# Optimization experiments

Measured on AMD Instinct MI355X. Metric: run time of the kernel, lower is better.

## Reference

```python
import jax, jax.numpy as jnp
import numpy as np

GRID_SIZE = 5
SPLINE_ORDER = 3
IN_FEAT = 320   # 32 * 10
OUT_FEAT = 2048 # 32 * 64
BN_EPS = 1e-3


def make_grid():
    # efficient-kan grid buffer: (in_features, grid_size + 2*spline_order + 1)
    h = 2.0 / GRID_SIZE  # grid_range = [-1, 1]
    g = jnp.arange(-SPLINE_ORDER, GRID_SIZE + SPLINE_ORDER + 1, dtype=jnp.float32) * h - 1.0
    return jnp.broadcast_to(g, (IN_FEAT, g.shape[0]))  # (320, 12)


def b_splines(x, grid):
    # x: (B, In) -> bases: (B, In, grid_size + spline_order)
    x = x[..., None]  # (B, In, 1)
    bases = ((x >= grid[:, :-1]) & (x < grid[:, 1:])).astype(x.dtype)
    for k in range(1, SPLINE_ORDER + 1):
        left = (x - grid[:, : -(k + 1)]) / (grid[:, k:-1] - grid[:, : -(k + 1)])
        right = (grid[:, k + 1:] - x) / (grid[:, k + 1:] - grid[:, 1:-k])
        bases = left * bases[..., :-1] + right * bases[..., 1:]
    return bases


def setup_inputs() -> dict:
    key = jax.random.key(0)
    ks = jax.random.split(key, 8)
    N = 40000
    inputs = jax.random.normal(ks[0], (N, 32, 10), dtype=jnp.float32)
    linear_w = jax.random.normal(ks[1], (64, 10), dtype=jnp.float32) * 0.1
    base_weight = jax.random.normal(ks[2], (OUT_FEAT, IN_FEAT), dtype=jnp.float32) * 0.02
    spline_weight = jax.random.normal(ks[3], (OUT_FEAT, IN_FEAT, GRID_SIZE + SPLINE_ORDER), dtype=jnp.float32) * 0.02
    spline_scaler = jax.random.normal(ks[4], (OUT_FEAT, IN_FEAT), dtype=jnp.float32) * 0.1 + 1.0
    bn_gamma = jax.random.normal(ks[5], (64,), dtype=jnp.float32) * 0.1 + 1.0
    bn_beta = jax.random.normal(ks[6], (64,), dtype=jnp.float32) * 0.1
    bn_mean = jnp.zeros((64,), dtype=jnp.float32)
    bn_var = jax.random.uniform(ks[7], (64,), dtype=jnp.float32, minval=0.5, maxval=1.5)
    return {
        "inputs": inputs,
        "linear_w": linear_w,
        "base_weight": base_weight,
        "spline_weight": spline_weight,
        "spline_scaler": spline_scaler,
        "bn_gamma": bn_gamma,
        "bn_beta": bn_beta,
        "bn_mean": bn_mean,
        "bn_var": bn_var,
    }


def reference(inputs, linear_w, base_weight, spline_weight, spline_scaler,
              bn_gamma, bn_beta, bn_mean, bn_var):
    N = inputs.shape[0]
    # plain linear path: (N, 32, 10) -> (N, 32, 64). (The torch chunking over
    # self.part is mathematically identical to one matmul.)
    x_linear = jnp.einsum('npi,oi->npo', inputs, linear_w)
    # KAN path on flattened pillars: (N, 320)
    xk = inputs.reshape(N, IN_FEAT)
    grid = make_grid()
    base_out = jnp.matmul(jax.nn.silu(xk), base_weight.T)  # (N, 2048)
    bases = b_splines(xk, grid)  # (N, 320, 8)
    scaled_spline_w = (spline_weight * spline_scaler[..., None]).reshape(OUT_FEAT, -1)
    spline_out = jnp.matmul(bases.reshape(N, -1), scaled_spline_w.T)  # (N, 2048)
    x_kan = (base_out + spline_out).reshape(N, 32, 64)
    x = x_linear + x_kan
    # BatchNorm1d over the channel (last) dim, inference mode, eps=1e-3
    inv_std = jax.lax.rsqrt(bn_var + BN_EPS)
    x = (x - bn_mean) * (inv_std * bn_gamma) + bn_beta
    x = jax.nn.relu(x)
    x_max = jnp.max(x, axis=1, keepdims=True)  # (N, 1, 64)
    x_rep = jnp.broadcast_to(x_max, x.shape)   # repeat over 32 points
    return jnp.concatenate([x, x_rep], axis=2)  # (N, 32, 128)
```

## Files before the change

kernel.cpp:

```cpp
#include <hip/hip_runtime.h>
#include <cstdint>
#include <math.h>

#define IN_FEAT 320
#define OUT_FEAT 2048
#define NB 8
#define KSIL 320
#define KTOT 2880
#define BM 128
#define BN 128
#define BK 32
#define LDA 40
#define BN_EPS 1e-3f
#define A_OFF ((size_t)16 << 20)

typedef __bf16 bf16;
typedef __attribute__((ext_vector_type(8))) __bf16 bf16x8;
typedef __attribute__((ext_vector_type(4))) float f32x4;

__device__ __forceinline__ void bspline8(float xv, float* b) {
    float xc = (xv + 2.2f) * 2.5f;
    float cf = floorf(xc);
    int c = (int)cf;
    float t = xc - cf;
    float omt = 1.0f - t;
    float t2 = t * t, t3 = t2 * t;
    float w0 = omt * omt * omt * (1.0f / 6.0f);
    float w1 = (3.0f * t3 - 6.0f * t2 + 4.0f) * (1.0f / 6.0f);
    float w2 = (-3.0f * t3 + 3.0f * t2 + 3.0f * t + 1.0f) * (1.0f / 6.0f);
    float w3 = t3 * (1.0f / 6.0f);
    if (xc < 0.0f) { w0 = w1 = w2 = w3 = 0.0f; }
#pragma unroll
    for (int j = 0; j < 8; ++j) {
        int d = c - j;
        b[j] = (d == 3) ? w0 : (d == 2) ? w1 : (d == 1) ? w2 : (d == 0) ? w3 : 0.0f;
    }
}

__device__ __forceinline__ bf16x8 pack8(const float* f) {
    bf16x8 v;
#pragma unroll
    for (int j = 0; j < 8; ++j) v[j] = (bf16)f[j];
    return v;
}

__device__ __forceinline__ void gl2lds16(const bf16* g, bf16* l) {
    __builtin_amdgcn_global_load_lds(
        (const __attribute__((address_space(1))) void*)g,
        (__attribute__((address_space(3))) void*)l, 16, 0, 0);
}

__global__ __launch_bounds__(256) void prep_w(const float* __restrict__ bw,
                                              const float* __restrict__ sw,
                                              const float* __restrict__ ss,
                                              bf16* __restrict__ W) {
    const int k = blockIdx.x * 256 + threadIdx.x;
    const int o = blockIdx.y;
    if (k >= KTOT) return;
    float w;
    if (k < KSIL) {
        w = bw[o * IN_FEAT + k];
    } else {
        const int s = k - KSIL;
        const int i = s >> 3, j = s & 7;
        w = sw[(o * IN_FEAT + i) * NB + j] * ss[o * IN_FEAT + i];
    }
    W[o * KTOT + k] = (bf16)w;
}

__global__ __launch_bounds__(256) void prep_a(const float* __restrict__ x,
                                              bf16* __restrict__ A, int total) {
    const int t = blockIdx.x * 256 + threadIdx.x;
    if (t >= total) return;
    const int row = t / IN_FEAT;
    const int f = t - row * IN_FEAT;
    const float xv = x[t];
    A[(size_t)row * KTOT + f] = (bf16)(xv / (1.0f + __expf(-xv)));
    float b[8];
    bspline8(xv, b);
    *(bf16x8*)&A[(size_t)row * KTOT + KSIL + f * 8] = pack8(b);
}

__global__ __launch_bounds__(256)
void pfn_gemm_ws(const float* __restrict__ x, const bf16* __restrict__ A,
                 const bf16* __restrict__ W, const float* __restrict__ lw,
                 const float* __restrict__ gamma, const float* __restrict__ beta,
                 const float* __restrict__ mean, const float* __restrict__ var,
                 float* __restrict__ out, int N, int nbx) {
    __shared__ bf16 As[BM * BK];
    __shared__ bf16 Bs[BN * BK];

    const int blk = blockIdx.x;
    const int sid = blk >> 9;
    const int t = blk & 511;
    const int by = t >> 5;
    const int bx = (sid << 5) + (t & 31);
    if (bx >= nbx) return;

    const int row0 = bx * BM;
    const int col0 = by * BN;
    const int tid = threadIdx.x;
    const int wave = tid >> 6;
    const int lane = tid & 63;
    const int wr = wave >> 1;
    const int wc = wave & 1;
    const int l15 = lane & 15;
    const int quad = lane >> 4;

    const int r0 = tid >> 2;
    const int s0 = tid & 3;
    const int g0 = s0 ^ ((r0 >> 1) & 3);
    const bf16* a0 = A + (size_t)(row0 + r0) * KTOT + g0 * 8;
    const bf16* a1 = a0 + (size_t)64 * KTOT;
    const bf16* b0 = W + (size_t)(col0 + r0) * KTOT + g0 * 8;
    const bf16* b1 = b0 + (size_t)64 * KTOT;
    bf16* lA0 = As + tid * 8;
    bf16* lA1 = As + (tid + 256) * 8;
    bf16* lB0 = Bs + tid * 8;
    bf16* lB1 = Bs + (tid + 256) * 8;

    const int sfr = quad ^ ((l15 >> 1) & 3);

    f32x4 acc[4][4] = {};

    for (int kc = 0; kc < KTOT; kc += BK) {
        __syncthreads();
        gl2lds16(a0 + kc, lA0);
        gl2lds16(a1 + kc, lA1);
        gl2lds16(b0 + kc, lB0);
        gl2lds16(b1 + kc, lB1);
        __syncthreads();
        bf16x8 af[4], bv[4];
#pragma unroll
        for (int i = 0; i < 4; ++i)
            af[i] = *(const bf16x8*)&As[(wr * 64 + i * 16 + l15) * BK + sfr * 8];
#pragma unroll
        for (int j = 0; j < 4; ++j)
            bv[j] = *(const bf16x8*)&Bs[(wc * 64 + j * 16 + l15) * BK + sfr * 8];
#pragma unroll
        for (int i = 0; i < 4; ++i)
#pragma unroll
            for (int j = 0; j < 4; ++j)
                acc[i][j] = __builtin_amdgcn_mfma_f32_16x16x32_bf16(af[i], bv[j],
                                                                   acc[i][j], 0, 0, 0);
    }

    const int p = by * 2 + wc;
    float sc[4], sh[4];
#pragma unroll
    for (int j = 0; j < 4; ++j) {
        const int c = j * 16 + l15;
        const float s = rsqrtf(var[c] + BN_EPS) * gamma[c];
        sc[j] = s;
        sh[j] = beta[c] - mean[c] * s;
    }
#pragma unroll
    for (int i = 0; i < 4; ++i) {
#pragma unroll
        for (int reg = 0; reg < 4; ++reg) {
            const int row = row0 + wr * 64 + i * 16 + quad * 4 + reg;
            if (row >= N) continue;
            float xq[10];
            const float* xp = &x[(size_t)row * IN_FEAT + p * 10];
#pragma unroll
            for (int q = 0; q < 10; ++q) xq[q] = xp[q];
#pragma unroll
            for (int j = 0; j < 4; ++j) {
                const int c = j * 16 + l15;
                float v = acc[i][j][reg];
#pragma unroll
                for (int q = 0; q < 10; ++q) v = fmaf(xq[q], lw[c * 10 + q], v);
                v = fmaxf(v * sc[j] + sh[j], 0.0f);
                out[((size_t)row * 32 + p) * 128 + c] = v;
            }
        }
    }
}

template <bool HASW>
__global__ __launch_bounds__(256)
void pfn_gemm(const float* __restrict__ x, const bf16* __restrict__ W,
              const float* __restrict__ bw, const float* __restrict__ sw,
              const float* __restrict__ ss, const float* __restrict__ lw,
              const float* __restrict__ gamma, const float* __restrict__ beta,
              const float* __restrict__ mean, const float* __restrict__ var,
              float* __restrict__ out, int N) {
    __shared__ bf16 As[BM * LDA];
    __shared__ bf16 Bs[BN * LDA];
    const int tid = threadIdx.x;
    const int row0 = blockIdx.x * BM;
    const int col0 = blockIdx.y * BN;
    const int wave = tid >> 6;
    const int lane = tid & 63;
    const int wr = wave >> 1;
    const int wc = wave & 1;
    const int l15 = lane & 15;
    const int quad = lane >> 4;
    f32x4 acc[4][4] = {};
    auto stage_b = [&](int kc) {
        const int ol = tid >> 1;
        const int k0 = (tid & 1) * 16;
        if (HASW) {
            const bf16x8* src = (const bf16x8*)&W[(size_t)(col0 + ol) * KTOT + kc + k0];
            *(bf16x8*)&Bs[ol * LDA + k0] = src[0];
            *(bf16x8*)&Bs[ol * LDA + k0 + 8] = src[1];
        } else {
            const int o = col0 + ol;
#pragma unroll
            for (int u = 0; u < 16; ++u) {
                const int gk = kc + k0 + u;
                float w;
                if (gk < KSIL) {
                    w = bw[o * IN_FEAT + gk];
                } else {
                    const int s = gk - KSIL;
                    const int i = s >> 3, j = s & 7;
                    w = sw[(o * IN_FEAT + i) * NB + j] * ss[o * IN_FEAT + i];
                }
                Bs[ol * LDA + k0 + u] = (bf16)w;
            }
        }
    };
    auto mma_step = [&]() {
        bf16x8 af[4], bv[4];
#pragma unroll
        for (int i = 0; i < 4; ++i)
            af[i] = *(const bf16x8*)&As[(wr * 64 + i * 16 + l15) * LDA + quad * 8];
#pragma unroll
        for (int j = 0; j < 4; ++j)
            bv[j] = *(const bf16x8*)&Bs[(wc * 64 + j * 16 + l15) * LDA + quad * 8];
#pragma unroll
        for (int i = 0; i < 4; ++i)
#pragma unroll
            for (int j = 0; j < 4; ++j)
                acc[i][j] = __builtin_amdgcn_mfma_f32_16x16x32_bf16(af[i], bv[j],
                                                                   acc[i][j], 0, 0, 0);
    };
    for (int kc = 0; kc < KSIL; kc += BK) {
        __syncthreads();
        stage_b(kc);
        {
            const int r = tid >> 1;
            const int k0 = (tid & 1) * 16;
            const int row = row0 + r;
            float v[16];
            if (row < N) {
                const float* xp = &x[(size_t)row * IN_FEAT + kc + k0];
#pragma unroll
                for (int u = 0; u < 16; ++u) {
                    const float xv = xp[u];
                    v[u] = xv / (1.0f + __expf(-xv));
                }
            } else {
#pragma unroll
                for (int u = 0; u < 16; ++u) v[u] = 0.0f;
            }
            *(bf16x8*)&As[r * LDA + k0] = pack8(v);
            *(bf16x8*)&As[r * LDA + k0 + 8] = pack8(v + 8);
        }
        __syncthreads();
        mma_step();
    }
    for (int kc = KSIL; kc < KTOT; kc += BK) {
        __syncthreads();
        stage_b(kc);
        {
            const int i0 = (kc - KSIL) >> 3;
#pragma unroll
            for (int s = 0; s < 2; ++s) {
                const int task = tid + s * 256;
                const int r = task >> 2;
                const int f = task & 3;
                const int row = row0 + r;
                float b[8];
                if (row < N) {
                    bspline8(x[(size_t)row * IN_FEAT + i0 + f], b);
                } else {
#pragma unroll
                    for (int j = 0; j < 8; ++j) b[j] = 0.0f;
                }
                *(bf16x8*)&As[r * LDA + f * 8] = pack8(b);
            }
        }
        __syncthreads();
        mma_step();
    }
    const int p = blockIdx.y * 2 + wc;
    float sc[4], sh[4];
#pragma unroll
    for (int j = 0; j < 4; ++j) {
        const int c = j * 16 + l15;
        const float s = rsqrtf(var[c] + BN_EPS) * gamma[c];
        sc[j] = s;
        sh[j] = beta[c] - mean[c] * s;
    }
#pragma unroll
    for (int i = 0; i < 4; ++i) {
#pragma unroll
        for (int reg = 0; reg < 4; ++reg) {
            const int row = row0 + wr * 64 + i * 16 + quad * 4 + reg;
            if (row >= N) continue;
            float xq[10];
            const float* xp = &x[(size_t)row * IN_FEAT + p * 10];
#pragma unroll
            for (int q = 0; q < 10; ++q) xq[q] = xp[q];
#pragma unroll
            for (int j = 0; j < 4; ++j) {
                const int c = j * 16 + l15;
                float v = acc[i][j][reg];
#pragma unroll
                for (int q = 0; q < 10; ++q) v = fmaf(xq[q], lw[c * 10 + q], v);
                v = fmaxf(v * sc[j] + sh[j], 0.0f);
                out[((size_t)row * 32 + p) * 128 + c] = v;
            }
        }
    }
}

__global__ __launch_bounds__(256) void pfn_maxcat(float* __restrict__ out, int N) {
    const int n = blockIdx.x;
    const int c = threadIdx.x & 63;
    const int g = threadIdx.x >> 6;
    __shared__ float red[4][64];
    float m = 0.0f;
    for (int pp = g; pp < 32; pp += 4)
        m = fmaxf(m, out[((size_t)n * 32 + pp) * 128 + c]);
    red[g][c] = m;
    __syncthreads();
    m = fmaxf(fmaxf(red[0][c], red[1][c]), fmaxf(red[2][c], red[3][c]));
    for (int pp = g; pp < 32; pp += 4)
        out[((size_t)n * 32 + pp) * 128 + 64 + c] = m;
}

extern "C" void kernel_launch(void* const* d_in, const int* in_sizes, int n_in,
                              void* d_out, int out_size, void* d_ws, size_t ws_size,
                              hipStream_t stream) {
    const float* x     = (const float*)d_in[0];
    const float* lw    = (const float*)d_in[1];
    const float* bw    = (const float*)d_in[2];
    const float* sw    = (const float*)d_in[3];
    const float* ss    = (const float*)d_in[4];
    const float* gamma = (const float*)d_in[5];
    const float* beta  = (const float*)d_in[6];
    const float* mean  = (const float*)d_in[7];
    const float* var   = (const float*)d_in[8];
    float* out = (float*)d_out;

    const int N = in_sizes[0] / IN_FEAT;
    const int nbx = (N + BM - 1) / BM;
    const size_t w_bytes = (size_t)OUT_FEAT * KTOT * sizeof(bf16);
    const size_t a_bytes = (size_t)nbx * BM * KTOT * sizeof(bf16);

    if (ws_size >= A_OFF + a_bytes) {
        bf16* W = (bf16*)d_ws;
        bf16* A = (bf16*)((char*)d_ws + A_OFF);
        prep_w<<<dim3((KTOT + 255) / 256, OUT_FEAT), 256, 0, stream>>>(bw, sw, ss, W);
        prep_a<<<(N * IN_FEAT + 255) / 256, 256, 0, stream>>>(x, A, N * IN_FEAT);
        const int supers = (nbx + 31) / 32;
        pfn_gemm_ws<<<supers * 512, 256, 0, stream>>>(x, A, W, lw, gamma, beta,
                                                      mean, var, out, N, nbx);
    } else if (ws_size >= w_bytes) {
        bf16* W = (bf16*)d_ws;
        prep_w<<<dim3((KTOT + 255) / 256, OUT_FEAT), 256, 0, stream>>>(bw, sw, ss, W);
        pfn_gemm<true><<<dim3(nbx, OUT_FEAT / BN), 256, 0, stream>>>(
            x, W, bw, sw, ss, lw, gamma, beta, mean, var, out, N);
    } else {
        pfn_gemm<false><<<dim3(nbx, OUT_FEAT / BN), 256, 0, stream>>>(
            x, nullptr, bw, sw, ss, lw, gamma, beta, mean, var, out, N);
    }
    pfn_maxcat<<<N, 256, 0, stream>>>(out, N);
}
```

Before: 1.697 ms.

## Enlarge GEMM tile to 256x128 with 512 threads and vectorize prep/maxcat kernels

The workspace GEMM moves from 128x128 tiles with 256 threads to 256-row tiles with 512 threads (8 waves), so each B tile is reused across twice as many rows and the B-side global traffic per output is halved. prep_w and prep_a now process 8 elements per thread with vector stores, and the max-concat kernel handles 16 pillars per block using float4 loads instead of a shared-memory reduction. The larger tile halves the number of row blocks and changes the block-to-data mapping, which risks occupancy loss and wave-quantization effects. The epilogue's wave-to-output indexing is hidden, so its correctness with 8 waves cannot be checked.

Result: faster. 1.582 ms (-6.8%).

```diff
diff --git a/kernel.cpp b/kernel.cpp
--- a/kernel.cpp
+++ b/kernel.cpp
@@ -7,6 +7,8 @@
 #define NB 8
 #define KSIL 320
 #define KTOT 2880
+#define BM1 256
+#define BN1 128
 #define BM 128
 #define BN 128
 #define BK 32
@@ -54,41 +56,56 @@
                                               const float* __restrict__ sw,
                                               const float* __restrict__ ss,
                                               bf16* __restrict__ W) {
-    const int k = blockIdx.x * 256 + threadIdx.x;
-    const int o = blockIdx.y;
-    if (k >= KTOT) return;
-    float w;
-    if (k < KSIL) {
-        w = bw[o * IN_FEAT + k];
+    const int t = blockIdx.x * 256 + threadIdx.x;
+    if (t >= OUT_FEAT * (KTOT / 8)) return;
+    const int o = t / (KTOT / 8);
+    const int m = t - o * (KTOT / 8);
+    const int k0 = m * 8;
+    float w[8];
+    if (k0 < KSIL) {
+        const float* p = &bw[o * IN_FEAT + k0];
+#pragma unroll
+        for (int u = 0; u < 8; ++u) w[u] = p[u];
     } else {
-        const int s = k - KSIL;
-        const int i = s >> 3, j = s & 7;
-        w = sw[(o * IN_FEAT + i) * NB + j] * ss[o * IN_FEAT + i];
-    }
-    W[o * KTOT + k] = (bf16)w;
+        const int i = (k0 - KSIL) >> 3;
+        const float s = ss[o * IN_FEAT + i];
+        const float* p = &sw[(o * IN_FEAT + i) * NB];
+#pragma unroll
+        for (int u = 0; u < 8; ++u) w[u] = p[u] * s;
+    }
+    *(bf16x8*)&W[(size_t)o * KTOT + k0] = pack8(w);
 }
 
 __global__ __launch_bounds__(256) void prep_a(const float* __restrict__ x,
-                                              bf16* __restrict__ A, int total) {
+                                              bf16* __restrict__ A, int total8) {
     const int t = blockIdx.x * 256 + threadIdx.x;
-    if (t >= total) return;
-    const int row = t / IN_FEAT;
-    const int f = t - row * IN_FEAT;
-    const float xv = x[t];
-    A[(size_t)row * KTOT + f] = (bf16)(xv / (1.0f + __expf(-xv)));
-    float b[8];
-    bspline8(xv, b);
-    *(bf16x8*)&A[(size_t)row * KTOT + KSIL + f * 8] = pack8(b);
-}
-
-__global__ __launch_bounds__(256)
+    if (t >= total8) return;
+    const int row = t / (IN_FEAT / 8);
+    const int f0 = (t - row * (IN_FEAT / 8)) * 8;
+    const float4 v0 = *(const float4*)&x[(size_t)row * IN_FEAT + f0];
+    const float4 v1 = *(const float4*)&x[(size_t)row * IN_FEAT + f0 + 4];
+    float xv[8] = {v0.x, v0.y, v0.z, v0.w, v1.x, v1.y, v1.z, v1.w};
+    float sil[8];
+#pragma unroll
+    for (int u = 0; u < 8; ++u) sil[u] = xv[u] / (1.0f + __expf(-xv[u]));
+    bf16* ar = A + (size_t)row * KTOT;
+    *(bf16x8*)&ar[f0] = pack8(sil);
+#pragma unroll
+    for (int u = 0; u < 8; ++u) {
+        float b[8];
+        bspline8(xv[u], b);
+        *(bf16x8*)&ar[KSIL + (f0 + u) * 8] = pack8(b);
+    }
+}
+
+__global__ __launch_bounds__(512)
 void pfn_gemm_ws(const float* __restrict__ x, const bf16* __restrict__ A,
                  const bf16* __restrict__ W, const float* __restrict__ lw,
                  const float* __restrict__ gamma, const float* __restrict__ beta,
                  const float* __restrict__ mean, const float* __restrict__ var,
                  float* __restrict__ out, int N, int nbx) {
-    __shared__ bf16 As[BM * BK];
-    __shared__ bf16 Bs[BN * BK];
+    __shared__ bf16 As[BM1 * BK];
+    __shared__ bf16 Bs[BN1 * BK];
 
     const int blk = blockIdx.x;
     const int sid = blk >> 9;
@@ -97,8 +114,8 @@
     const int bx = (sid << 5) + (t & 31);
     if (bx >= nbx) return;
 
-    const int row0 = bx * BM;
-    const int col0 = by * BN;
+    const int row0 = bx * BM1;
+    const int col0 = by * BN1;
     const int tid = threadIdx.x;
     const int wave = tid >> 6;
     const int lane = tid & 63;
@@ -111,13 +128,11 @@
     const int s0 = tid & 3;
     const int g0 = s0 ^ ((r0 >> 1) & 3);
     const bf16* a0 = A + (size_t)(row0 + r0) * KTOT + g0 * 8;
-    const bf16* a1 = a0 + (size_t)64 * KTOT;
+    const bf16* a1 = a0 + (size_t)128 * KTOT;
     const bf16* b0 = W + (size_t)(col0 + r0) * KTOT + g0 * 8;
-    const bf16* b1 = b0 + (size_t)64 * KTOT;
     bf16* lA0 = As + tid * 8;
-    bf16* lA1 = As + (tid + 256) * 8;
+    bf16* lA1 = As + (tid + 512) * 8;
     bf16* lB0 = Bs + tid * 8;
-    bf16* lB1 = Bs + (tid + 256) * 8;
 
     const int sfr = quad ^ ((l15 >> 1) & 3);
 
@@ -128,7 +143,6 @@
         gl2lds16(a0 + kc, lA0);
         gl2lds16(a1 + kc, lA1);
         gl2lds16(b0 + kc, lB0);
-        gl2lds16(b1 + kc, lB1);
         __syncthreads();
         bf16x8 af[4], bv[4];
 #pragma unroll
@@ -318,18 +332,22 @@
 }
 
 __global__ __launch_bounds__(256) void pfn_maxcat(float* __restrict__ out, int N) {
-    const int n = blockIdx.x;
-    const int c = threadIdx.x & 63;
-    const int g = threadIdx.x >> 6;
-    __shared__ float red[4][64];
-    float m = 0.0f;
-    for (int pp = g; pp < 32; pp += 4)
-        m = fmaxf(m, out[((size_t)n * 32 + pp) * 128 + c]);
-    red[g][c] = m;
-    __syncthreads();
-    m = fmaxf(fmaxf(red[0][c], red[1][c]), fmaxf(red[2][c], red[3][c]));
-    for (int pp = g; pp < 32; pp += 4)
-        out[((size_t)n * 32 + pp) * 128 + 64 + c] = m;
+    const int n = blockIdx.x * 16 + (threadIdx.x >> 4);
+    const int q = threadIdx.x & 15;
+    if (n >= N) return;
+    float* base = out + (size_t)n * 32 * 128 + q * 4;
+    f32x4 m = {0.0f, 0.0f, 0.0f, 0.0f};
+#pragma unroll
+    for (int pp = 0; pp < 32; ++pp) {
+        const f32x4 v = *(const f32x4*)&base[pp * 128];
+        m[0] = fmaxf(m[0], v[0]);
+        m[1] = fmaxf(m[1], v[1]);
+        m[2] = fmaxf(m[2], v[2]);
+        m[3] = fmaxf(m[3], v[3]);
+    }
+#pragma unroll
+    for (int pp = 0; pp < 32; ++pp)
+        *(f32x4*)&base[pp * 128 + 64] = m;
 }
 
 extern "C" void kernel_launch(void* const* d_in, const int* in_sizes, int n_in,
@@ -347,26 +365,27 @@
     float* out = (float*)d_out;
 
     const int N = in_sizes[0] / IN_FEAT;
-    const int nbx = (N + BM - 1) / BM;
+    const int nbx = (N + BM1 - 1) / BM1;
     const size_t w_bytes = (size_t)OUT_FEAT * KTOT * sizeof(bf16);
-    const size_t a_bytes = (size_t)nbx * BM * KTOT * sizeof(bf16);
+    const size_t a_bytes = (size_t)nbx * BM1 * KTOT * sizeof(bf16);
 
     if (ws_size >= A_OFF + a_bytes) {
         bf16* W = (bf16*)d_ws;
         bf16* A = (bf16*)((char*)d_ws + A_OFF);
-        prep_w<<<dim3((KTOT + 255) / 256, OUT_FEAT), 256, 0, stream>>>(bw, sw, ss, W);
-        prep_a<<<(N * IN_FEAT + 255) / 256, 256, 0, stream>>>(x, A, N * IN_FEAT);
+        prep_w<<<(OUT_FEAT * (KTOT / 8) + 255) / 256, 256, 0, stream>>>(bw, sw, ss, W);
+        const int total8 = N * (IN_FEAT / 8);
+        prep_a<<<(total8 + 255) / 256, 256, 0, stream>>>(x, A, total8);
         const int supers = (nbx + 31) / 32;
-        pfn_gemm_ws<<<supers * 512, 256, 0, stream>>>(x, A, W, lw, gamma, beta,
+        pfn_gemm_ws<<<supers * 512, 512, 0, stream>>>(x, A, W, lw, gamma, beta,
                                                       mean, var, out, N, nbx);
     } else if (ws_size >= w_bytes) {
         bf16* W = (bf16*)d_ws;
-        prep_w<<<dim3((KTOT + 255) / 256, OUT_FEAT), 256, 0, stream>>>(bw, sw, ss, W);
-        pfn_gemm<true><<<dim3(nbx, OUT_FEAT / BN), 256, 0, stream>>>(
+        prep_w<<<(OUT_FEAT * (KTOT / 8) + 255) / 256, 256, 0, stream>>>(bw, sw, ss, W);
+        pfn_gemm<true><<<dim3((N + BM - 1) / BM, OUT_FEAT / BN), 256, 0, stream>>>(
             x, W, bw, sw, ss, lw, gamma, beta, mean, var, out, N);
     } else {
-        pfn_gemm<false><<<dim3(nbx, OUT_FEAT / BN), 256, 0, stream>>>(
+        pfn_gemm<false><<<dim3((N + BM - 1) / BM, OUT_FEAT / BN), 256, 0, stream>>>(
             x, nullptr, bw, sw, ss, lw, gamma, beta, mean, var, out, N);
     }
-    pfn_maxcat<<<N, 256, 0, stream>>>(out, N);
-}
+    pfn_maxcat<<<(N + 15) / 16, 256, 0, stream>>>(out, N);
+}
```
